# Kernel tuning notes

Hardware: AMD Instinct MI355X
Metric: run time of the kernel (lower is better)

Reference implementation:

```python
import jax, jax.numpy as jnp
import numpy as np

V, D, H, L = 6000, 512, 512, 2
B, S, T = 32, 6, 32
PAD, SOS, EOS1, EOS2 = 0, 1, 2, 3
EPS = 1e-5


def layer_norm(x, g, b):
    m = x.mean(-1, keepdims=True)
    v = ((x - m) ** 2).mean(-1, keepdims=True)
    return (x - m) / jnp.sqrt(v + EPS) * g + b


def lstm_stack_step(x, h, c, Wih_list, Whh, bias):
    # x: [B, in], h/c: [L, B, H]; pytorch gate order i,f,g,o
    hs, cs = [], []
    inp = x
    for l in range(L):
        gates = inp @ Wih_list[l].T + h[l] @ Whh[l].T + bias[l]
        i, f, g, o = jnp.split(gates, 4, axis=-1)
        c2 = jax.nn.sigmoid(f) * c[l] + jax.nn.sigmoid(i) * jnp.tanh(g)
        h2 = jax.nn.sigmoid(o) * jnp.tanh(c2)
        hs.append(h2); cs.append(c2); inp = h2
    return jnp.stack(hs), jnp.stack(cs)


def run_encoder(tokens, h, c, enc_emb, enc_Wih, enc_Whh, enc_b, ln_g, ln_b):
    emb = enc_emb[tokens]  # [B,T,D]
    def step(carry, x_t):
        hh, cc = lstm_stack_step(x_t, carry[0], carry[1], [enc_Wih[0], enc_Wih[1]], enc_Whh, enc_b)
        return (hh, cc), hh[-1]
    (h, c), outs = jax.lax.scan(step, (h, c), emb.transpose(1, 0, 2))
    outs = layer_norm(outs.transpose(1, 0, 2), ln_g, ln_b)  # [B,T,H]
    return outs, h, c


def decode_sentence(dec_tokens, h, c, enc_outs, mask, dec_emb, att_W, att_b, att_v,
                    dec_Wih0, dec_Wih1, dec_Whh, dec_b, ln_g, ln_b, fc_W, fc_b):
    emb = dec_emb[dec_tokens]  # [B,T,D]
    def step(carry, x_t):
        h, c = carry
        if enc_outs is None:
            context = jnp.zeros((x_t.shape[0], H), x_t.dtype)
        else:
            q = jnp.broadcast_to(h[-1][:, None, :], enc_outs.shape)  # [B,T,H]
            e = jnp.tanh(jnp.concatenate([q, enc_outs], -1) @ att_W.T + att_b)
            scores = jnp.where(mask, -1e9, e @ att_v)  # [B,T]
            a = jax.nn.softmax(scores, axis=1)
            context = jnp.einsum('bt,bth->bh', a, enc_outs)
        x = jnp.concatenate([x_t, context], -1)
        h, c = lstm_stack_step(x, h, c, [dec_Wih0, dec_Wih1], dec_Whh, dec_b)
        return (h, c), h[-1]
    (h, c), outs = jax.lax.scan(step, (h, c), emb.transpose(1, 0, 2))
    outs = layer_norm(outs, ln_g, ln_b)  # [T,B,H]
    logits = outs @ fc_W.T + fc_b        # [T,B,V]
    return logits.transpose(1, 0, 2), h, c


def setup_inputs() -> dict:
    key = jax.random.key(0)
    ks = jax.random.split(key, 20)
    w = lambda k, *s: jax.random.normal(k, s, jnp.float32) * 0.02
    enc_emb = w(ks[0], V, D).at[PAD].set(0.0)
    dec_emb = w(ks[1], V, D).at[PAD].set(0.0)
    return {
        'inputs': jax.random.randint(ks[2], (B, S, T), 0, V),
        'targets': jax.random.randint(ks[3], (B, S - 1, T), 0, V),
        'enc_emb': enc_emb,
        'enc_Wih': w(ks[4], L, 4 * H, D),
        'enc_Whh': w(ks[5], L, 4 * H, H),
        'enc_b': jnp.zeros((L, 4 * H), jnp.float32),
        'enc_ln_g': jnp.ones((H,), jnp.float32),
        'enc_ln_b': jnp.zeros((H,), jnp.float32),
        'dec_emb': dec_emb,
        'att_W': w(ks[6], H, 2 * H),
        'att_b': jnp.zeros((H,), jnp.float32),
        'att_v': w(ks[7], H),
        'dec_Wih0': w(ks[8], 4 * H, D + H),
        'dec_Wih1': w(ks[9], 4 * H, H),
        'dec_Whh': w(ks[10], L, 4 * H, H),
        'dec_b': jnp.zeros((L, 4 * H), jnp.float32),
        'dec_ln_g': jnp.ones((H,), jnp.float32),
        'dec_ln_b': jnp.zeros((H,), jnp.float32),
        'fc_W': w(ks[11], V, H),
        'fc_b': jnp.zeros((V,), jnp.float32),
    }


def reference(inputs, targets, enc_emb, enc_Wih, enc_Whh, enc_b, enc_ln_g, enc_ln_b,
              dec_emb, att_W, att_b, att_v, dec_Wih0, dec_Wih1, dec_Whh, dec_b,
              dec_ln_g, dec_ln_b, fc_W, fc_b):
    # teacher_force_ratio = 1.0 (deterministic), dropout in eval mode
    dec_h = jnp.zeros((L, B, H), jnp.float32)
    dec_c = jnp.zeros((L, B, H), jnp.float32)
    enc_h = jnp.zeros((L, B, H), jnp.float32)
    enc_c = jnp.zeros((L, B, H), jnp.float32)
    enc_outs = None
    mask = jnp.zeros((B, T), bool)
    sent_logits = []
    for s in range(S):
        tok = inputs[:, 0, :] if s == 0 else targets[:, s - 1, :]
        dec_in = jnp.concatenate([jnp.full((B, 1), SOS, tok.dtype), tok[:, :-1]], 1)
        logits, dec_h, dec_c = decode_sentence(dec_in, dec_h, dec_c, enc_outs, mask,
                                               dec_emb, att_W, att_b, att_v,
                                               dec_Wih0, dec_Wih1, dec_Whh, dec_b,
                                               dec_ln_g, dec_ln_b, fc_W, fc_b)
        if s > 0:
            sent_logits.append(logits)
        # mask for the NEXT sentence: positions strictly after the first EOS
        is_eos = (tok == EOS1) | (tok == EOS2)
        seen = jnp.cumsum(is_eos.astype(jnp.int32), axis=1) > 0
        mask = jnp.concatenate([jnp.zeros((B, 1), bool), seen[:, :-1]], 1)
        if s < S - 1:
            enc_outs, enc_h, enc_c = run_encoder(tok, enc_h, enc_c, enc_emb, enc_Wih,
                                                 enc_Whh, enc_b, enc_ln_g, enc_ln_b)
    return jnp.stack(sent_logits, axis=1)  # [B, S-1, T, V]
```

## Files before the change

kernel.cpp:

```cpp
#include <hip/hip_runtime.h>

typedef unsigned short u16;
typedef __attribute__((ext_vector_type(8))) short bf8;
typedef __attribute__((ext_vector_type(4))) float f4;
typedef __attribute__((ext_vector_type(4))) unsigned int u32x4;

struct Params {
  const int* inputs; const int* targets;
  const void *enc_emb, *enc_Wih, *enc_Whh, *enc_bias, *enc_ln_g, *enc_ln_b;
  const void *dec_emb, *att_W, *att_b, *att_v;
  const void *dec_Wih0, *dec_Wih1, *dec_Whh, *dec_bias, *dec_ln_g, *dec_ln_b;
  const void *fc_W, *fc_b;
  void* out;
};

__device__ __align__(16) u16 gb_enc_emb[3072000];
__device__ __align__(16) u16 gb_dec_emb[3072000];
__device__ __align__(16) u16 gb_enc_Wih[2097152];
__device__ __align__(16) u16 gb_enc_Whh[2097152];
__device__ __align__(16) u16 gb_dec_Wih0[2097152];
__device__ __align__(16) u16 gb_dec_Wih1[1048576];
__device__ __align__(16) u16 gb_dec_Whh[2097152];
__device__ __align__(16) u16 gb_att_W[524288];
__device__ __align__(16) u16 gb_fc_W[3072000];
__device__ float gc_enc_bias[4096], gc_dec_bias[4096];
__device__ float gc_enc_ln_g[512], gc_enc_ln_b[512], gc_dec_ln_g[512], gc_dec_ln_b[512];
__device__ float gc_att_b[512], gc_att_v[512], gc_fc_b[6000];

__device__ __align__(16) u16 g_Hdec[4 * 32 * 512];
__device__ __align__(16) u16 g_Henc[4 * 32 * 512];
__device__ __align__(16) u16 g_ctx[32 * 512];
__device__ __align__(16) u16 g_outsb[1024 * 512];
__device__ __align__(16) u16 g_lnouts[1024 * 512];
__device__ __align__(16) u16 g_encraw[1024 * 512];
__device__ __align__(16) u16 g_encouts[2][1024 * 512];
__device__ __align__(16) u16 g_encpart[2][1024 * 512];
__device__ __align__(16) float g_Cdec[2 * 32 * 512];
__device__ __align__(16) float g_Cenc[2 * 32 * 512];
__device__ __align__(16) float g_pqp[32 * 32 * 512];
__device__ int g_masks[6 * 32 * 32];
__device__ int g_dtoks[6 * 32 * 32];
__device__ int g_etoks[5 * 32 * 32];

__device__ __forceinline__ float b2f(u16 u) { union { unsigned i; float f; } v; v.i = ((unsigned)u) << 16; return v.f; }
__device__ __forceinline__ u16 f2b(float f) {
  union { float f; unsigned i; } v; v.f = f;
  unsigned x = v.i;
  return (u16)((x + 0x7fffu + ((x >> 16) & 1u)) >> 16);
}
__device__ __forceinline__ float sigf(float x) { return 1.f / (1.f + __expf(-x)); }
__device__ __forceinline__ float tanhf_(float x) { float e = __expf(2.f * x); return 1.f - 2.f / (e + 1.f); }

__device__ __forceinline__ bool is_f32(const Params& P) {
  return *(const unsigned*)P.enc_ln_g == 0x3F800000u;
}

struct Acc2 { f4 lo, hi; };

__device__ __forceinline__ void mm_seg(Acc2& a, const u16* A, const u16* Wp, int ldW, int K, int lane) {
  const int n = lane & 15, q = lane >> 4;
  const u16* a0 = A + n * 512 + q * 8;
  const u16* a1 = a0 + 16 * 512;
  const u16* bp = Wp + n * ldW + q * 8;
  for (int k = 0; k < K; k += 32) {
    bf8 va0 = *(const bf8*)(a0 + k);
    bf8 va1 = *(const bf8*)(a1 + k);
    bf8 vb  = *(const bf8*)(bp + k);
    a.lo = __builtin_amdgcn_mfma_f32_16x16x32_bf16(va0, vb, a.lo, 0, 0, 0);
    a.hi = __builtin_amdgcn_mfma_f32_16x16x32_bf16(va1, vb, a.hi, 0, 0, 0);
  }
}

__device__ __forceinline__ void mm_tok(Acc2& a, const u16* emb, const int* toks,
                                       const u16* Wp, int ldW, int lane) {
  const int n = lane & 15, q = lane >> 4;
  const u16* a0 = emb + (size_t)toks[n] * 512 + q * 8;
  const u16* a1 = emb + (size_t)toks[n + 16] * 512 + q * 8;
  const u16* bp = Wp + n * ldW + q * 8;
  for (int k = 0; k < 512; k += 32) {
    bf8 va0 = *(const bf8*)(a0 + k);
    bf8 va1 = *(const bf8*)(a1 + k);
    bf8 vb  = *(const bf8*)(bp + k);
    a.lo = __builtin_amdgcn_mfma_f32_16x16x32_bf16(va0, vb, a.lo, 0, 0, 0);
    a.hi = __builtin_amdgcn_mfma_f32_16x16x32_bf16(va1, vb, a.hi, 0, 0, 0);
  }
}

__device__ __forceinline__ void lstm_phase(char* sbuf, int u, int lane, int wave, int tid,
    const u16* emb, const int* toks,
    const u16* A1c,
    const u16* W1, int ldW1,
    const u16* A2, const u16* W2, int ldW2, int k2off,
    const u16* A3, const u16* W3,
    const float* bias, float* Cst, u16* Hout,
    u16* Xtra, int xmode, int t,
    bool do_pqp, const u16* attW, float* pqp)
{
  float* gl = (float*)sbuf;
  float* hl = (float*)(sbuf + 4 * 32 * 17 * 4);
  const int n = lane & 15, q = lane >> 4;
  const int colbase = wave * 512 + u * 16;
  float bv = bias[colbase + n];
  f4 bi = { bv, bv, bv, bv };
  Acc2 acc; acc.lo = bi; acc.hi = bi;
  if (toks) mm_tok(acc, emb, toks, W1 + colbase * ldW1, ldW1, lane);
  else      mm_seg(acc, A1c, W1 + colbase * ldW1, ldW1, 512, lane);
  if (A2) mm_seg(acc, A2, W2 + colbase * ldW2 + k2off, ldW2, 512, lane);
  mm_seg(acc, A3, W3 + colbase * 512, 512, 512, lane);
#pragma unroll
  for (int r = 0; r < 4; r++) {
    gl[(wave * 32 + q * 4 + r) * 17 + n]      = acc.lo[r];
    gl[(wave * 32 + 16 + q * 4 + r) * 17 + n] = acc.hi[r];
  }
  __syncthreads();
  for (int p = tid; p < 512; p += 256) {
    int b = p >> 4, nn = p & 15, hc = u * 16 + nn;
    float iv = gl[(0 * 32 + b) * 17 + nn];
    float fv = gl[(1 * 32 + b) * 17 + nn];
    float gv = gl[(2 * 32 + b) * 17 + nn];
    float ov = gl[(3 * 32 + b) * 17 + nn];
    float c2 = sigf(fv) * Cst[b * 512 + hc] + sigf(iv) * tanhf_(gv);
    float h2 = sigf(ov) * tanhf_(c2);
    Cst[b * 512 + hc] = c2;
    u16 hb = f2b(h2);
    Hout[b * 512 + hc] = hb;
    if (xmode == 1)      Xtra[(t * 32 + b) * 512 + hc] = hb;
    else if (xmode == 2) Xtra[(b * 32 + t) * 512 + hc] = hb;
    if (do_pqp) hl[b * 16 + nn] = h2;
  }
  if (do_pqp) {
    __syncthreads();
    for (int h = tid; h < 512; h += 256) {
      float wl[16];
#pragma unroll
      for (int j = 0; j < 16; j++) wl[j] = b2f(attW[h * 1024 + u * 16 + j]);
      for (int b = 0; b < 32; b++) {
        float s = 0.f;
#pragma unroll
        for (int j = 0; j < 16; j++) s += hl[b * 16 + j] * wl[j];
        pqp[(u * 32 + b) * 512 + h] = s;
      }
    }
  }
}


__global__ void __launch_bounds__(256) k_conv(Params P)
{
  const bool f32 = is_f32(P);
  int c = blockIdx.x * 256 + threadIdx.x;
  const void* src; u16* dst;
  if (c < 384000)                 { src = P.enc_emb;  dst = gb_enc_emb;  }
  else if ((c -= 384000) < 384000){ src = P.dec_emb;  dst = gb_dec_emb;  }
  else if ((c -= 384000) < 262144){ src = P.enc_Wih;  dst = gb_enc_Wih;  }
  else if ((c -= 262144) < 262144){ src = P.enc_Whh;  dst = gb_enc_Whh;  }
  else if ((c -= 262144) < 262144){ src = P.dec_Wih0; dst = gb_dec_Wih0; }
  else if ((c -= 262144) < 131072){ src = P.dec_Wih1; dst = gb_dec_Wih1; }
  else if ((c -= 131072) < 262144){ src = P.dec_Whh;  dst = gb_dec_Whh;  }
  else if ((c -= 262144) < 65536) { src = P.att_W;    dst = gb_att_W;    }
  else                            { c -= 65536; src = P.fc_W; dst = gb_fc_W; }
  if (f32) {
    const float* s = (const float*)src + (size_t)c * 8;
    union { u32x4 v; u16 o[8]; } u;
#pragma unroll
    for (int j = 0; j < 8; j++) u.o[j] = f2b(s[j]);
    *(u32x4*)(dst + (size_t)c * 8) = u.v;
  } else {
    ((u32x4*)dst)[c] = ((const u32x4*)src)[c];
  }
}

__global__ void __launch_bounds__(256) k_conv_small(Params P)
{
  const bool f32 = is_f32(P);
  int i = blockIdx.x * 256 + threadIdx.x;
  const void* src; float* dst;
  if (i < 4096)                 { src = P.enc_bias; dst = gc_enc_bias; }
  else if ((i -= 4096) < 4096)  { src = P.dec_bias; dst = gc_dec_bias; }
  else if ((i -= 4096) < 512)   { src = P.enc_ln_g; dst = gc_enc_ln_g; }
  else if ((i -= 512) < 512)    { src = P.enc_ln_b; dst = gc_enc_ln_b; }
  else if ((i -= 512) < 512)    { src = P.dec_ln_g; dst = gc_dec_ln_g; }
  else if ((i -= 512) < 512)    { src = P.dec_ln_b; dst = gc_dec_ln_b; }
  else if ((i -= 512) < 512)    { src = P.att_b;    dst = gc_att_b;    }
  else if ((i -= 512) < 512)    { src = P.att_v;    dst = gc_att_v;    }
  else if ((i -= 512) < 6000)   { src = P.fc_b;     dst = gc_fc_b;     }
  else return;
  dst[i] = f32 ? ((const float*)src)[i] : b2f(((const u16*)src)[i]);
}

__global__ void __launch_bounds__(256) k_setup(Params P)
{
  const int gtid = blockIdx.x * 256 + threadIdx.x;
  if (gtid < 6144) {
    int s = gtid >> 10, rem = gtid & 1023, t = rem >> 5, b = rem & 31;
    int tok = (t == 0) ? 1
            : ((s == 0) ? P.inputs[b * 192 + (t - 1)] : P.targets[b * 160 + (s - 1) * 32 + (t - 1)]);
    g_dtoks[gtid] = tok;
  } else if (gtid < 6144 + 5120) {
    int gi = gtid - 6144;
    int s = gi >> 10, rem = gi & 1023, t = rem >> 5, b = rem & 31;
    g_etoks[gi] = (s == 0) ? P.inputs[b * 192 + t] : P.targets[b * 160 + (s - 1) * 32 + t];
  }
  if (blockIdx.x >= 64 && blockIdx.x < 224 && threadIdx.x == 0) {
    int w = blockIdx.x - 64;
    int s = 1 + (w >> 5), b = w & 31;
    int seen = 0;
    g_masks[(s * 32 + b) * 32 + 0] = 0;
    for (int t2 = 1; t2 < 32; t2++) {
      int tk = (s == 1) ? P.inputs[b * 192 + (t2 - 1)] : P.targets[b * 160 + (s - 2) * 32 + (t2 - 1)];
      seen |= (tk == 2 || tk == 3) ? 1 : 0;
      g_masks[(s * 32 + b) * 32 + t2] = seen;
    }
  }
  u32x4 z = { 0u, 0u, 0u, 0u };
  if (gtid < 8192)  ((u32x4*)g_Hdec)[gtid] = z;
  if (gtid >= 8192 && gtid < 16384) ((u32x4*)g_Henc)[gtid - 8192] = z;
  if (gtid >= 16384 && gtid < 18432) ((u32x4*)g_ctx)[gtid - 16384] = z;
  if (gtid >= 18432 && gtid < 26624) ((u32x4*)g_Cdec)[gtid - 18432] = z;
  if (gtid >= 26624 && gtid < 34816) ((u32x4*)g_Cenc)[gtid - 26624] = z;
}

__global__ void __launch_bounds__(256) k_att(Params P, int s)
{
  __shared__ float sm[512 + 32 + 32];
  float* qp = sm; float* sc = qp + 512; float* av = sc + 32;
  const int b = blockIdx.x, tid = threadIdx.x;
  const int lane = tid & 63, wave = tid >> 6;
  const int sprev = (s & 1) ^ 1;
  const u16* ep_prev = g_encpart[sprev];
  const u16* eo_prev = g_encouts[sprev];

  for (int h = tid; h < 512; h += 256) {
    float ssum = 0.f;
#pragma unroll 4
    for (int u = 0; u < 32; u++) ssum += g_pqp[(u * 32 + b) * 512 + h];
    qp[h] = ssum;
  }
  __syncthreads();
  for (int tt = wave; tt < 32; tt += 4) {
    float part = 0.f;
    for (int h = lane; h < 512; h += 64)
      part += tanhf_(qp[h] + b2f(ep_prev[(b * 32 + tt) * 512 + h])) * gc_att_v[h];
#pragma unroll
    for (int off = 32; off; off >>= 1) part += __shfl_xor(part, off, 64);
    if (lane == 0) sc[tt] = g_masks[(s * 32 + b) * 32 + tt] ? -1e9f : fminf(fmaxf(part, -1e30f), 1e30f);
  }
  __syncthreads();
  if (wave == 0) {
    float v = (lane < 32) ? sc[lane] : -3e38f;
    float m = v;
#pragma unroll
    for (int off = 32; off; off >>= 1) m = fmaxf(m, __shfl_xor(m, off, 64));
    float e = (lane < 32) ? __expf(v - m) : 0.f;
    float ssum = e;
#pragma unroll
    for (int off = 32; off; off >>= 1) ssum += __shfl_xor(ssum, off, 64);
    if (lane < 32) av[lane] = e / ssum;
  }
  __syncthreads();
  for (int h = tid; h < 512; h += 256) {
    float ssum = 0.f;
#pragma unroll 4
    for (int tt = 0; tt < 32; tt++) ssum += av[tt] * b2f(eo_prev[(b * 32 + tt) * 512 + h]);
    g_ctx[b * 512 + h] = f2b(ssum);
  }
}

__global__ void __launch_bounds__(256) k_p0(Params P, int s, int t)
{
  __shared__ char sbuf[4 * 32 * 17 * 4 + 32 * 16 * 4];
  const int blk = blockIdx.x, tid = threadIdx.x;
  const int lane = tid & 63, wave = tid >> 6;
  const int gstep = s * 32 + t, si = gstep & 1, so = si ^ 1;
  if (blk < 32) {
    lstm_phase(sbuf, blk, lane, wave, tid,
      gb_dec_emb, g_dtoks + gstep * 32, nullptr, gb_dec_Wih0, 1024,
      (s > 0) ? g_ctx : nullptr, gb_dec_Wih0, 1024, 512,
      g_Hdec + (si * 2 + 0) * 16384, gb_dec_Whh,
      gc_dec_bias, g_Cdec, g_Hdec + (so * 2 + 0) * 16384,
      nullptr, 0, t, false, nullptr, nullptr);
  } else {
    lstm_phase(sbuf, blk - 32, lane, wave, tid,
      gb_enc_emb, g_etoks + gstep * 32, nullptr, gb_enc_Wih, 512,
      nullptr, nullptr, 0, 0,
      g_Henc + (si * 2 + 0) * 16384, gb_enc_Whh,
      gc_enc_bias, g_Cenc, g_Henc + (so * 2 + 0) * 16384,
      nullptr, 0, t, false, nullptr, nullptr);
  }
}

__global__ void __launch_bounds__(256) k_p1(Params P, int s, int t, int dp)
{
  __shared__ char sbuf[4 * 32 * 17 * 4 + 32 * 16 * 4];
  const int blk = blockIdx.x, tid = threadIdx.x;
  const int lane = tid & 63, wave = tid >> 6;
  const int gstep = s * 32 + t, si = gstep & 1, so = si ^ 1;
  if (blk < 32) {
    lstm_phase(sbuf, blk, lane, wave, tid,
      nullptr, nullptr, g_Hdec + (so * 2 + 0) * 16384, gb_dec_Wih1, 512,
      nullptr, nullptr, 0, 0,
      g_Hdec + (si * 2 + 1) * 16384, gb_dec_Whh + 1048576,
      gc_dec_bias + 2048, g_Cdec + 16384, g_Hdec + (so * 2 + 1) * 16384,
      g_outsb, 1, t, dp != 0, gb_att_W, g_pqp);
  } else {
    lstm_phase(sbuf, blk - 32, lane, wave, tid,
      nullptr, nullptr, g_Henc + (so * 2 + 0) * 16384, gb_enc_Wih + 1048576, 512,
      nullptr, nullptr, 0, 0,
      g_Henc + (si * 2 + 1) * 16384, gb_enc_Whh + 1048576,
      gc_enc_bias + 2048, g_Cenc + 16384, g_Henc + (so * 2 + 1) * 16384,
      g_encraw, 2, t, false, nullptr, nullptr);
  }
}

__global__ void __launch_bounds__(256) k_ln(Params P, int s)
{
  const int blk = blockIdx.x, tid = threadIdx.x;
  const int lane = tid & 63, wave = tid >> 6;
  const u16* in; u16* out; const float *gw, *bw; int blkrel;
  if (blk < 128) {
    if (s == 0) return;
    in = g_outsb; out = g_lnouts; gw = gc_dec_ln_g; bw = gc_dec_ln_b; blkrel = blk;
  } else {
    if (s >= 5) return;
    in = g_encraw; out = g_encouts[s & 1]; gw = gc_enc_ln_g; bw = gc_enc_ln_b; blkrel = blk - 128;
  }
#pragma unroll
  for (int rr = 0; rr < 2; rr++) {
    int row = blkrel * 8 + wave * 2 + rr;
    const u16* x = in + row * 512 + lane * 8;
    float xs[8]; float sm = 0.f, sq = 0.f;
#pragma unroll
    for (int j = 0; j < 8; j++) { xs[j] = b2f(x[j]); sm += xs[j]; sq += xs[j] * xs[j]; }
#pragma unroll
    for (int off = 32; off; off >>= 1) { sm += __shfl_xor(sm, off, 64); sq += __shfl_xor(sq, off, 64); }
    float mean = sm * (1.f / 512.f);
    float var = fmaxf(sq * (1.f / 512.f) - mean * mean, 0.f);
    float rstd = rsqrtf(var + 1e-5f);
    u16* o = out + row * 512 + lane * 8;
#pragma unroll
    for (int j = 0; j < 8; j++) {
      int k = lane * 8 + j;
      o[j] = f2b((xs[j] - mean) * rstd * gw[k] + bw[k]);
    }
  }
}

__global__ void __launch_bounds__(256) k_fc(Params P, int s)
{
  __shared__ char sbuf[65536];
  const int blk = blockIdx.x, tid = threadIdx.x;
  const int lane = tid & 63, wave = tid >> 6;
  const int n = lane & 15, q = lane >> 4;
  if (blk < 192) {
    if (s == 0) return;
    const bool f32o = is_f32(P);
    u16* As = (u16*)sbuf;
    int mc = blk / 12, ncc = blk % 12;
    int mrow0 = mc * 64;
    for (int idx = tid; idx < 64 * 64; idx += 256) {
      int row = idx >> 6, ch = idx & 63;
      int phys = ch ^ (row & 7);
      *(u32x4*)(As + (row * 64 + phys) * 8) = *(const u32x4*)(g_lnouts + (mrow0 + row) * 512 + ch * 8);
    }
    __syncthreads();
    f4 acc[4][8];
#pragma unroll
    for (int j = 0; j < 8; j++) {
      int c = ncc * 512 + wave * 128 + j * 16 + n;
      float bv = (c < 6000) ? gc_fc_b[c] : 0.f;
      f4 bi = { bv, bv, bv, bv };
#pragma unroll
      for (int mt = 0; mt < 4; mt++) acc[mt][j] = bi;
    }
    for (int kt = 0; kt < 16; kt++) {
      bf8 a[4];
#pragma unroll
      for (int mt = 0; mt < 4; mt++) {
        int row = mt * 16 + n;
        int ch = kt * 4 + q;
        int phys = ch ^ (row & 7);
        a[mt] = *(const bf8*)(As + (row * 64 + phys) * 8);
      }
#pragma unroll
      for (int j = 0; j < 8; j++) {
        int c = ncc * 512 + wave * 128 + j * 16 + n;
        int brow = (c < 6000) ? c : 5999;
        bf8 vb = *(const bf8*)(gb_fc_W + brow * 512 + kt * 32 + q * 8);
#pragma unroll
        for (int mt = 0; mt < 4; mt++)
          acc[mt][j] = __builtin_amdgcn_mfma_f32_16x16x32_bf16(a[mt], vb, acc[mt][j], 0, 0, 0);
      }
    }
#pragma unroll
    for (int j = 0; j < 8; j++) {
      int c = ncc * 512 + wave * 128 + j * 16 + n;
      if (c < 6000) {
#pragma unroll
        for (int mt = 0; mt < 4; mt++) {
#pragma unroll
          for (int r = 0; r < 4; r++) {
            int rix = mrow0 + mt * 16 + q * 4 + r;
            int tt = rix >> 5, b = rix & 31;
            size_t oidx = (size_t)((b * 5 + (s - 1)) * 32 + tt) * 6000 + c;
            float v = acc[mt][j][r];
            if (f32o) ((float*)P.out)[oidx] = v;
            else      ((u16*)P.out)[oidx] = f2b(v);
          }
        }
      }
    }
  } else {
    if (s >= 5) return;
    const u16* eo_cur = g_encouts[s & 1];
    u16* ep_cur = g_encpart[s & 1];
    int wg = blk - 192;
    int rc = wg >> 3, cc = wg & 7;
    int nbase = cc * 64 + wave * 16;
    float bv = gc_att_b[nbase + n];
#pragma unroll
    for (int mt = 0; mt < 4; mt++) {
      int rowbase = rc * 128 + mt * 32;
      f4 bi = { bv, bv, bv, bv };
      Acc2 acc; acc.lo = bi; acc.hi = bi;
      mm_seg(acc, eo_cur + rowbase * 512, gb_att_W + nbase * 1024 + 512, 1024, 512, lane);
#pragma unroll
      for (int r = 0; r < 4; r++) {
        int row = rowbase + q * 4 + r;
        ep_cur[row * 512 + nbase + n]        = f2b(acc.lo[r]);
        ep_cur[(row + 16) * 512 + nbase + n] = f2b(acc.hi[r]);
      }
    }
  }
}

extern "C" void kernel_launch(void* const* d_in, const int* in_sizes, int n_in,
                              void* d_out, int out_size, void* d_ws, size_t ws_size,
                              hipStream_t stream) {
  Params P;
  P.inputs   = (const int*)d_in[0];
  P.targets  = (const int*)d_in[1];
  P.enc_emb  = d_in[2];
  P.enc_Wih  = d_in[3];
  P.enc_Whh  = d_in[4];
  P.enc_bias = d_in[5];
  P.enc_ln_g = d_in[6];
  P.enc_ln_b = d_in[7];
  P.dec_emb  = d_in[8];
  P.att_W    = d_in[9];
  P.att_b    = d_in[10];
  P.att_v    = d_in[11];
  P.dec_Wih0 = d_in[12];
  P.dec_Wih1 = d_in[13];
  P.dec_Whh  = d_in[14];
  P.dec_bias = d_in[15];
  P.dec_ln_g = d_in[16];
  P.dec_ln_b = d_in[17];
  P.fc_W     = d_in[18];
  P.fc_b     = d_in[19];
  P.out = d_out;

  hipLaunchKernelGGL(k_conv, dim3(9364), dim3(256), 0, stream, P);
  hipLaunchKernelGGL(k_conv_small, dim3(68), dim3(256), 0, stream, P);
  hipLaunchKernelGGL(k_setup, dim3(256), dim3(256), 0, stream, P);

  for (int s = 0; s < 6; s++) {
    const bool enc = (s < 5);
    for (int t = 0; t < 32; t++) {
      if (s > 0) hipLaunchKernelGGL(k_att, dim3(32), dim3(256), 0, stream, P, s);
      hipLaunchKernelGGL(k_p0, dim3(enc ? 64 : 32), dim3(256), 0, stream, P, s, t);
      int dp = ((s > 0 && t < 31) || (t == 31 && s < 5)) ? 1 : 0;
      hipLaunchKernelGGL(k_p1, dim3(enc ? 64 : 32), dim3(256), 0, stream, P, s, t, dp);
    }
    hipLaunchKernelGGL(k_ln, dim3(256), dim3(256), 0, stream, P, s);
    hipLaunchKernelGGL(k_fc, dim3(256), dim3(256), 0, stream, P, s);
  }
}
```

Baseline: 12.35 ms.

## Replace per-step kernel launches with persistent kernel using grid barriers

Merges the roughly 500 per-timestep attention and LSTM-layer launches into one persistent 64-block kernel that syncs through a custom atomic grid barrier. It also reorders the work so the encoder layer-0 step overlaps the decoder attention step, and the encoder layer-1 step overlaps decoder layer 0. Decoder outputs for all sentences are buffered so the layernorm and FC projection run once at the end as two batched kernels. This removes launch overhead and serialization on the long recurrent chain. The cost is spin-wait barrier latency and the assumption that all 64 blocks are resident at once.

```diff
diff --git a/kernel.cpp b/kernel.cpp
--- a/kernel.cpp
+++ b/kernel.cpp
@@ -30,8 +30,8 @@
 __device__ __align__(16) u16 g_Hdec[4 * 32 * 512];
 __device__ __align__(16) u16 g_Henc[4 * 32 * 512];
 __device__ __align__(16) u16 g_ctx[32 * 512];
-__device__ __align__(16) u16 g_outsb[1024 * 512];
-__device__ __align__(16) u16 g_lnouts[1024 * 512];
+__device__ __align__(16) u16 g_outsb5[5 * 1024 * 512];
+__device__ __align__(16) u16 g_lnouts5[5 * 1024 * 512];
 __device__ __align__(16) u16 g_encraw[1024 * 512];
 __device__ __align__(16) u16 g_encouts[2][1024 * 512];
 __device__ __align__(16) u16 g_encpart[2][1024 * 512];
@@ -42,6 +42,9 @@
 __device__ int g_dtoks[6 * 32 * 32];
 __device__ int g_etoks[5 * 32 * 32];
 
+__device__ unsigned g_flags[64 * 16];
+__device__ unsigned g_gen;
+
 __device__ __forceinline__ float b2f(u16 u) { union { unsigned i; float f; } v; v.i = ((unsigned)u) << 16; return v.f; }
 __device__ __forceinline__ u16 f2b(float f) {
   union { float f; unsigned i; } v; v.f = f;
@@ -53,6 +56,29 @@
 
 __device__ __forceinline__ bool is_f32(const Params& P) {
   return *(const unsigned*)P.enc_ln_g == 0x3F800000u;
+}
+
+__device__ __forceinline__ void gridbar(int blk, int tid, unsigned& g) {
+  g += 1;
+  __syncthreads();
+  if (blk == 0) {
+    if (tid >= 1 && tid < 64) {
+      while (__hip_atomic_load(&g_flags[tid * 16], __ATOMIC_RELAXED, __HIP_MEMORY_SCOPE_AGENT) != g)
+        __builtin_amdgcn_s_sleep(1);
+    }
+    __syncthreads();
+    __builtin_amdgcn_fence(__ATOMIC_ACQUIRE, "agent");
+    if (tid == 0)
+      __hip_atomic_store(&g_gen, g, __ATOMIC_RELEASE, __HIP_MEMORY_SCOPE_AGENT);
+  } else {
+    if (tid == 0) {
+      __hip_atomic_store(&g_flags[blk * 16], g, __ATOMIC_RELEASE, __HIP_MEMORY_SCOPE_AGENT);
+      while (__hip_atomic_load(&g_gen, __ATOMIC_RELAXED, __HIP_MEMORY_SCOPE_AGENT) != g)
+        __builtin_amdgcn_s_sleep(1);
+    }
+    __syncthreads();
+    __builtin_amdgcn_fence(__ATOMIC_ACQUIRE, "agent");
+  }
 }
 
 struct Acc2 { f4 lo, hi; };
@@ -144,6 +170,49 @@
   }
 }
 
+__device__ __forceinline__ void att_dev(char* sbufc, int b, int s, int lane, int wave, int tid)
+{
+  float* qp = (float*)sbufc; float* sc = qp + 512; float* av = sc + 32;
+  const int sprev = (s & 1) ^ 1;
+  const u16* ep_prev = g_encpart[sprev];
+  const u16* eo_prev = g_encouts[sprev];
+
+  for (int h = tid; h < 512; h += 256) {
+    float ssum = 0.f;
+#pragma unroll 4
+    for (int u = 0; u < 32; u++) ssum += g_pqp[(u * 32 + b) * 512 + h];
+    qp[h] = ssum;
+  }
+  __syncthreads();
+  for (int tt = wave; tt < 32; tt += 4) {
+    float part = 0.f;
+    for (int h = lane; h < 512; h += 64)
+      part += tanhf_(qp[h] + b2f(ep_prev[(b * 32 + tt) * 512 + h])) * gc_att_v[h];
+#pragma unroll
+    for (int off = 32; off; off >>= 1) part += __shfl_xor(part, off, 64);
+    if (lane == 0) sc[tt] = g_masks[(s * 32 + b) * 32 + tt] ? -1e9f : fminf(fmaxf(part, -1e30f), 1e30f);
+  }
+  __syncthreads();
+  if (wave == 0) {
+    float v = (lane < 32) ? sc[lane] : -3e38f;
+    float m = v;
+#pragma unroll
+    for (int off = 32; off; off >>= 1) m = fmaxf(m, __shfl_xor(m, off, 64));
+    float e = (lane < 32) ? __expf(v - m) : 0.f;
+    float ssum = e;
+#pragma unroll
+    for (int off = 32; off; off >>= 1) ssum += __shfl_xor(ssum, off, 64);
+    if (lane < 32) av[lane] = e / ssum;
+  }
+  __syncthreads();
+  for (int h = tid; h < 512; h += 256) {
+    float ssum = 0.f;
+#pragma unroll 4
+    for (int tt = 0; tt < 32; tt++) ssum += av[tt] * b2f(eo_prev[(b * 32 + tt) * 512 + h]);
+    g_ctx[b * 512 + h] = f2b(ssum);
+  }
+}
+
 
 __global__ void __launch_bounds__(256) k_conv(Params P)
 {
@@ -220,114 +289,115 @@
   if (gtid >= 26624 && gtid < 34816) ((u32x4*)g_Cenc)[gtid - 26624] = z;
 }
 
-__global__ void __launch_bounds__(256) k_att(Params P, int s)
-{
-  __shared__ float sm[512 + 32 + 32];
-  float* qp = sm; float* sc = qp + 512; float* av = sc + 32;
-  const int b = blockIdx.x, tid = threadIdx.x;
-  const int lane = tid & 63, wave = tid >> 6;
-  const int sprev = (s & 1) ^ 1;
-  const u16* ep_prev = g_encpart[sprev];
-  const u16* eo_prev = g_encouts[sprev];
-
-  for (int h = tid; h < 512; h += 256) {
-    float ssum = 0.f;
-#pragma unroll 4
-    for (int u = 0; u < 32; u++) ssum += g_pqp[(u * 32 + b) * 512 + h];
-    qp[h] = ssum;
-  }
-  __syncthreads();
-  for (int tt = wave; tt < 32; tt += 4) {
-    float part = 0.f;
-    for (int h = lane; h < 512; h += 64)
-      part += tanhf_(qp[h] + b2f(ep_prev[(b * 32 + tt) * 512 + h])) * gc_att_v[h];
-#pragma unroll
-    for (int off = 32; off; off >>= 1) part += __shfl_xor(part, off, 64);
-    if (lane == 0) sc[tt] = g_masks[(s * 32 + b) * 32 + tt] ? -1e9f : fminf(fmaxf(part, -1e30f), 1e30f);
-  }
-  __syncthreads();
-  if (wave == 0) {
-    float v = (lane < 32) ? sc[lane] : -3e38f;
-    float m = v;
-#pragma unroll
-    for (int off = 32; off; off >>= 1) m = fmaxf(m, __shfl_xor(m, off, 64));
-    float e = (lane < 32) ? __expf(v - m) : 0.f;
-    float ssum = e;
-#pragma unroll
-    for (int off = 32; off; off >>= 1) ssum += __shfl_xor(ssum, off, 64);
-    if (lane < 32) av[lane] = e / ssum;
-  }
-  __syncthreads();
-  for (int h = tid; h < 512; h += 256) {
-    float ssum = 0.f;
-#pragma unroll 4
-    for (int tt = 0; tt < 32; tt++) ssum += av[tt] * b2f(eo_prev[(b * 32 + tt) * 512 + h]);
-    g_ctx[b * 512 + h] = f2b(ssum);
-  }
-}
-
-__global__ void __launch_bounds__(256) k_p0(Params P, int s, int t)
+__global__ void __launch_bounds__(256) k_persist(Params P)
 {
   __shared__ char sbuf[4 * 32 * 17 * 4 + 32 * 16 * 4];
   const int blk = blockIdx.x, tid = threadIdx.x;
   const int lane = tid & 63, wave = tid >> 6;
-  const int gstep = s * 32 + t, si = gstep & 1, so = si ^ 1;
-  if (blk < 32) {
-    lstm_phase(sbuf, blk, lane, wave, tid,
-      gb_dec_emb, g_dtoks + gstep * 32, nullptr, gb_dec_Wih0, 1024,
-      (s > 0) ? g_ctx : nullptr, gb_dec_Wih0, 1024, 512,
-      g_Hdec + (si * 2 + 0) * 16384, gb_dec_Whh,
-      gc_dec_bias, g_Cdec, g_Hdec + (so * 2 + 0) * 16384,
-      nullptr, 0, t, false, nullptr, nullptr);
-  } else {
-    lstm_phase(sbuf, blk - 32, lane, wave, tid,
-      gb_enc_emb, g_etoks + gstep * 32, nullptr, gb_enc_Wih, 512,
-      nullptr, nullptr, 0, 0,
-      g_Henc + (si * 2 + 0) * 16384, gb_enc_Whh,
-      gc_enc_bias, g_Cenc, g_Henc + (so * 2 + 0) * 16384,
-      nullptr, 0, t, false, nullptr, nullptr);
-  }
-}
-
-__global__ void __launch_bounds__(256) k_p1(Params P, int s, int t, int dp)
-{
-  __shared__ char sbuf[4 * 32 * 17 * 4 + 32 * 16 * 4];
+  unsigned g = __hip_atomic_load(&g_gen, __ATOMIC_RELAXED, __HIP_MEMORY_SCOPE_AGENT);
+
+  for (int s = 0; s < 6; s++) {
+    for (int t = 0; t < 32; t++) {
+      const int gstep = s * 32 + t, si = gstep & 1, so = si ^ 1;
+      if (blk < 32) {
+        if (s < 5)
+          lstm_phase(sbuf, blk, lane, wave, tid,
+            gb_enc_emb, g_etoks + gstep * 32, nullptr, gb_enc_Wih, 512,
+            nullptr, nullptr, 0, 0,
+            g_Henc + (si * 2 + 0) * 16384, gb_enc_Whh,
+            gc_enc_bias, g_Cenc, g_Henc + (so * 2 + 0) * 16384,
+            nullptr, 0, t, false, nullptr, nullptr);
+      } else if (s > 0) {
+        att_dev(sbuf, blk - 32, s, lane, wave, tid);
+      }
+      gridbar(blk, tid, g);
+      if (blk < 32) {
+        if (s < 5)
+          lstm_phase(sbuf, blk, lane, wave, tid,
+            nullptr, nullptr, g_Henc + (so * 2 + 0) * 16384, gb_enc_Wih + 1048576, 512,
+            nullptr, nullptr, 0, 0,
+            g_Henc + (si * 2 + 1) * 16384, gb_enc_Whh + 1048576,
+            gc_enc_bias + 2048, g_Cenc + 16384, g_Henc + (so * 2 + 1) * 16384,
+            g_encraw, 2, t, false, nullptr, nullptr);
+      } else {
+        lstm_phase(sbuf, blk - 32, lane, wave, tid,
+          gb_dec_emb, g_dtoks + gstep * 32, nullptr, gb_dec_Wih0, 1024,
+          (s > 0) ? g_ctx : nullptr, gb_dec_Wih0, 1024, 512,
+          g_Hdec + (si * 2 + 0) * 16384, gb_dec_Whh,
+          gc_dec_bias, g_Cdec, g_Hdec + (so * 2 + 0) * 16384,
+          nullptr, 0, t, false, nullptr, nullptr);
+      }
+      gridbar(blk, tid, g);
+      if (blk >= 32) {
+        int dp = ((s > 0 && t < 31) || (t == 31 && s < 5)) ? 1 : 0;
+        u16* outp = (s >= 1) ? (g_outsb5 + (size_t)(s - 1) * 524288) : nullptr;
+        lstm_phase(sbuf, blk - 32, lane, wave, tid,
+          nullptr, nullptr, g_Hdec + (so * 2 + 0) * 16384, gb_dec_Wih1, 512,
+          nullptr, nullptr, 0, 0,
+          g_Hdec + (si * 2 + 1) * 16384, gb_dec_Whh + 1048576,
+          gc_dec_bias + 2048, g_Cdec + 16384, g_Hdec + (so * 2 + 1) * 16384,
+          outp, outp ? 1 : 0, t, dp != 0, gb_att_W, g_pqp);
+      }
+      gridbar(blk, tid, g);
+    }
+    if (s < 5) {
+      {
+        u16* out = g_encouts[s & 1];
+#pragma unroll
+        for (int rr = 0; rr < 4; rr++) {
+          int row = blk * 16 + wave * 4 + rr;
+          const u16* x = g_encraw + row * 512 + lane * 8;
+          float xs[8]; float sm = 0.f, sq = 0.f;
+#pragma unroll
+          for (int j = 0; j < 8; j++) { xs[j] = b2f(x[j]); sm += xs[j]; sq += xs[j] * xs[j]; }
+#pragma unroll
+          for (int off = 32; off; off >>= 1) { sm += __shfl_xor(sm, off, 64); sq += __shfl_xor(sq, off, 64); }
+          float mean = sm * (1.f / 512.f);
+          float var = fmaxf(sq * (1.f / 512.f) - mean * mean, 0.f);
+          float rstd = rsqrtf(var + 1e-5f);
+          u16* o = out + row * 512 + lane * 8;
+#pragma unroll
+          for (int j = 0; j < 8; j++) {
+            int k = lane * 8 + j;
+            o[j] = f2b((xs[j] - mean) * rstd * gc_enc_ln_g[k] + gc_enc_ln_b[k]);
+          }
+        }
+      }
+      gridbar(blk, tid, g);
+      {
+        const u16* eo_cur = g_encouts[s & 1];
+        u16* ep_cur = g_encpart[s & 1];
+        const int n = lane & 15, q = lane >> 4;
+        int rc = blk >> 3, cc = blk & 7;
+        int nbase = cc * 64 + wave * 16;
+        float bv = gc_att_b[nbase + n];
+#pragma unroll
+        for (int mt = 0; mt < 4; mt++) {
+          int rowbase = rc * 128 + mt * 32;
+          f4 bi = { bv, bv, bv, bv };
+          Acc2 acc; acc.lo = bi; acc.hi = bi;
+          mm_seg(acc, eo_cur + rowbase * 512, gb_att_W + nbase * 1024 + 512, 1024, 512, lane);
+#pragma unroll
+          for (int r = 0; r < 4; r++) {
+            int row = rowbase + q * 4 + r;
+            ep_cur[row * 512 + nbase + n]        = f2b(acc.lo[r]);
+            ep_cur[(row + 16) * 512 + nbase + n] = f2b(acc.hi[r]);
+          }
+        }
+      }
+      gridbar(blk, tid, g);
+    }
+  }
+}
+
+__global__ void __launch_bounds__(256) k_ln_post(Params P)
+{
   const int blk = blockIdx.x, tid = threadIdx.x;
   const int lane = tid & 63, wave = tid >> 6;
-  const int gstep = s * 32 + t, si = gstep & 1, so = si ^ 1;
-  if (blk < 32) {
-    lstm_phase(sbuf, blk, lane, wave, tid,
-      nullptr, nullptr, g_Hdec + (so * 2 + 0) * 16384, gb_dec_Wih1, 512,
-      nullptr, nullptr, 0, 0,
-      g_Hdec + (si * 2 + 1) * 16384, gb_dec_Whh + 1048576,
-      gc_dec_bias + 2048, g_Cdec + 16384, g_Hdec + (so * 2 + 1) * 16384,
-      g_outsb, 1, t, dp != 0, gb_att_W, g_pqp);
-  } else {
-    lstm_phase(sbuf, blk - 32, lane, wave, tid,
-      nullptr, nullptr, g_Henc + (so * 2 + 0) * 16384, gb_enc_Wih + 1048576, 512,
-      nullptr, nullptr, 0, 0,
-      g_Henc + (si * 2 + 1) * 16384, gb_enc_Whh + 1048576,
-      gc_enc_bias + 2048, g_Cenc + 16384, g_Henc + (so * 2 + 1) * 16384,
-      g_encraw, 2, t, false, nullptr, nullptr);
-  }
-}
-
-__global__ void __launch_bounds__(256) k_ln(Params P, int s)
-{
-  const int blk = blockIdx.x, tid = threadIdx.x;
-  const int lane = tid & 63, wave = tid >> 6;
-  const u16* in; u16* out; const float *gw, *bw; int blkrel;
-  if (blk < 128) {
-    if (s == 0) return;
-    in = g_outsb; out = g_lnouts; gw = gc_dec_ln_g; bw = gc_dec_ln_b; blkrel = blk;
-  } else {
-    if (s >= 5) return;
-    in = g_encraw; out = g_encouts[s & 1]; gw = gc_enc_ln_g; bw = gc_enc_ln_b; blkrel = blk - 128;
-  }
 #pragma unroll
   for (int rr = 0; rr < 2; rr++) {
-    int row = blkrel * 8 + wave * 2 + rr;
-    const u16* x = in + row * 512 + lane * 8;
+    int row = blk * 8 + wave * 2 + rr;
+    const u16* x = g_outsb5 + (size_t)row * 512 + lane * 8;
     float xs[8]; float sm = 0.f, sq = 0.f;
 #pragma unroll
     for (int j = 0; j < 8; j++) { xs[j] = b2f(x[j]); sm += xs[j]; sq += xs[j] * xs[j]; }
@@ -336,98 +406,76 @@
     float mean = sm * (1.f / 512.f);
     float var = fmaxf(sq * (1.f / 512.f) - mean * mean, 0.f);
     float rstd = rsqrtf(var + 1e-5f);
-    u16* o = out + row * 512 + lane * 8;
+    u16* o = g_lnouts5 + (size_t)row * 512 + lane * 8;
 #pragma unroll
     for (int j = 0; j < 8; j++) {
       int k = lane * 8 + j;
-      o[j] = f2b((xs[j] - mean) * rstd * gw[k] + bw[k]);
-    }
-  }
-}
-
-__global__ void __launch_bounds__(256) k_fc(Params P, int s)
+      o[j] = f2b((xs[j] - mean) * rstd * gc_dec_ln_g[k] + gc_dec_ln_b[k]);
+    }
+  }
+}
+
+__global__ void __launch_bounds__(256) k_fc_post(Params P)
 {
   __shared__ char sbuf[65536];
-  const int blk = blockIdx.x, tid = threadIdx.x;
+  const int blk0 = blockIdx.x, tid = threadIdx.x;
+  const int sidx = blk0 / 192, blk = blk0 % 192;
   const int lane = tid & 63, wave = tid >> 6;
   const int n = lane & 15, q = lane >> 4;
-  if (blk < 192) {
-    if (s == 0) return;
-    const bool f32o = is_f32(P);
-    u16* As = (u16*)sbuf;
-    int mc = blk / 12, ncc = blk % 12;
-    int mrow0 = mc * 64;
-    for (int idx = tid; idx < 64 * 64; idx += 256) {
-      int row = idx >> 6, ch = idx & 63;
+  const bool f32o = is_f32(P);
+  const u16* lnin = g_lnouts5 + (size_t)sidx * 524288;
+  u16* As = (u16*)sbuf;
+  int mc = blk / 12, ncc = blk % 12;
+  int mrow0 = mc * 64;
+  for (int idx = tid; idx < 64 * 64; idx += 256) {
+    int row = idx >> 6, ch = idx & 63;
+    int phys = ch ^ (row & 7);
+    *(u32x4*)(As + (row * 64 + phys) * 8) = *(const u32x4*)(lnin + (size_t)(mrow0 + row) * 512 + ch * 8);
+  }
+  __syncthreads();
+  f4 acc[4][8];
+#pragma unroll
+  for (int j = 0; j < 8; j++) {
+    int c = ncc * 512 + wave * 128 + j * 16 + n;
+    float bv = (c < 6000) ? gc_fc_b[c] : 0.f;
+    f4 bi = { bv, bv, bv, bv };
+#pragma unroll
+    for (int mt = 0; mt < 4; mt++) acc[mt][j] = bi;
+  }
+  for (int kt = 0; kt < 16; kt++) {
+    bf8 a[4];
+#pragma unroll
+    for (int mt = 0; mt < 4; mt++) {
+      int row = mt * 16 + n;
+      int ch = kt * 4 + q;
       int phys = ch ^ (row & 7);
-      *(u32x4*)(As + (row * 64 + phys) * 8) = *(const u32x4*)(g_lnouts + (mrow0 + row) * 512 + ch * 8);
-    }
-    __syncthreads();
-    f4 acc[4][8];
+      a[mt] = *(const bf8*)(As + (row * 64 + phys) * 8);
+    }
 #pragma unroll
     for (int j = 0; j < 8; j++) {
       int c = ncc * 512 + wave * 128 + j * 16 + n;
-      float bv = (c < 6000) ? gc_fc_b[c] : 0.f;
-      f4 bi = { bv, bv, bv, bv };
-#pragma unroll
-      for (int mt = 0; mt < 4; mt++) acc[mt][j] = bi;
-    }
-    for (int kt = 0; kt < 16; kt++) {
-      bf8 a[4];
+      int brow = (c < 6000) ? c : 5999;
+      bf8 vb = *(const bf8*)(gb_fc_W + brow * 512 + kt * 32 + q * 8);
+#pragma unroll
+      for (int mt = 0; mt < 4; mt++)
+        acc[mt][j] = __builtin_amdgcn_mfma_f32_16x16x32_bf16(a[mt], vb, acc[mt][j], 0, 0, 0);
+    }
+  }
+#pragma unroll
+  for (int j = 0; j < 8; j++) {
+    int c = ncc * 512 + wave * 128 + j * 16 + n;
+    if (c < 6000) {
 #pragma unroll
       for (int mt = 0; mt < 4; mt++) {
-        int row = mt * 16 + n;
-        int ch = kt * 4 + q;
-        int phys = ch ^ (row & 7);
-        a[mt] = *(const bf8*)(As + (row * 64 + phys) * 8);
-      }
-#pragma unroll
-      for (int j = 0; j < 8; j++) {
-        int c = ncc * 512 + wave * 128 + j * 16 + n;
-        int brow = (c < 6000) ? c : 5999;
-        bf8 vb = *(const bf8*)(gb_fc_W + brow * 512 + kt * 32 + q * 8);
-#pragma unroll
-        for (int mt = 0; mt < 4; mt++)
-          acc[mt][j] = __builtin_amdgcn_mfma_f32_16x16x32_bf16(a[mt], vb, acc[mt][j], 0, 0, 0);
-      }
-    }
-#pragma unroll
-    for (int j = 0; j < 8; j++) {
-      int c = ncc * 512 + wave * 128 + j * 16 + n;
-      if (c < 6000) {
-#pragma unroll
-        for (int mt = 0; mt < 4; mt++) {
-#pragma unroll
-          for (int r = 0; r < 4; r++) {
-            int rix = mrow0 + mt * 16 + q * 4 + r;
-            int tt = rix >> 5, b = rix & 31;
-            size_t oidx = (size_t)((b * 5 + (s - 1)) * 32 + tt) * 6000 + c;
-            float v = acc[mt][j][r];
-            if (f32o) ((float*)P.out)[oidx] = v;
-            else      ((u16*)P.out)[oidx] = f2b(v);
-          }
+#pragma unroll
+        for (int r = 0; r < 4; r++) {
+          int rix = mrow0 + mt * 16 + q * 4 + r;
+          int tt = rix >> 5, b = rix & 31;
+          size_t oidx = (size_t)((b * 5 + sidx) * 32 + tt) * 6000 + c;
+          float v = acc[mt][j][r];
+          if (f32o) ((float*)P.out)[oidx] = v;
+          else      ((u16*)P.out)[oidx] = f2b(v);
         }
-      }
-    }
-  } else {
-    if (s >= 5) return;
-    const u16* eo_cur = g_encouts[s & 1];
-    u16* ep_cur = g_encpart[s & 1];
-    int wg = blk - 192;
-    int rc = wg >> 3, cc = wg & 7;
-    int nbase = cc * 64 + wave * 16;
-    float bv = gc_att_b[nbase + n];
-#pragma unroll
-    for (int mt = 0; mt < 4; mt++) {
-      int rowbase = rc * 128 + mt * 32;
-      f4 bi = { bv, bv, bv, bv };
-      Acc2 acc; acc.lo = bi; acc.hi = bi;
-      mm_seg(acc, eo_cur + rowbase * 512, gb_att_W + nbase * 1024 + 512, 1024, 512, lane);
-#pragma unroll
-      for (int r = 0; r < 4; r++) {
-        int row = rowbase + q * 4 + r;
-        ep_cur[row * 512 + nbase + n]        = f2b(acc.lo[r]);
-        ep_cur[(row + 16) * 512 + nbase + n] = f2b(acc.hi[r]);
       }
     }
   }
@@ -462,16 +510,7 @@
   hipLaunchKernelGGL(k_conv, dim3(9364), dim3(256), 0, stream, P);
   hipLaunchKernelGGL(k_conv_small, dim3(68), dim3(256), 0, stream, P);
   hipLaunchKernelGGL(k_setup, dim3(256), dim3(256), 0, stream, P);
-
-  for (int s = 0; s < 6; s++) {
-    const bool enc = (s < 5);
-    for (int t = 0; t < 32; t++) {
-      if (s > 0) hipLaunchKernelGGL(k_att, dim3(32), dim3(256), 0, stream, P, s);
-      hipLaunchKernelGGL(k_p0, dim3(enc ? 64 : 32), dim3(256), 0, stream, P, s, t);
-      int dp = ((s > 0 && t < 31) || (t == 31 && s < 5)) ? 1 : 0;
-      hipLaunchKernelGGL(k_p1, dim3(enc ? 64 : 32), dim3(256), 0, stream, P, s, t, dp);
-    }
-    hipLaunchKernelGGL(k_ln, dim3(256), dim3(256), 0, stream, P, s);
-    hipLaunchKernelGGL(k_fc, dim3(256), dim3(256), 0, stream, P, s);
-  }
-}
+  hipLaunchKernelGGL(k_persist, dim3(64), dim3(256), 0, stream, P);
+  hipLaunchKernelGGL(k_ln_post, dim3(640), dim3(256), 0, stream, P);
+  hipLaunchKernelGGL(k_fc_post, dim3(960), dim3(256), 0, stream, P);
+}
```

Measured after the change: 15.71 ms. 27.2% more time.
